# Kernel tuning notes

Measured on AMD Instinct MI355X. Metric: run time of the kernel, lower is better.

Reference implementation:

```python
import jax, jax.numpy as jnp
import numpy as np

CH = (64, 128, 256, 512)
KV = sum(CH)          # 960, kv_size = sum(channel_num)
EPS = 1e-5            # InstanceNorm2d default eps
SCALE = 1.0 / float(np.sqrt(KV))


def setup_inputs() -> dict:
    key = jax.random.key(0)
    ks = jax.random.split(key, 16)
    B, N = 16, 1024
    d = {}
    for i, c in enumerate(CH):
        d[f"emb{i+1}"] = jax.random.normal(ks[i], (B, N, c), jnp.float32)
    d["emb_all"] = jax.random.normal(ks[4], (B, N, KV), jnp.float32)
    for i, c in enumerate(CH):
        # two stacked query heads per branch, Linear weights [out,in]
        d[f"Wq{i+1}"] = jax.random.normal(ks[5 + i], (2, c, c), jnp.float32) * 0.05
        d[f"Wo{i+1}"] = jax.random.normal(ks[9 + i], (c, c), jnp.float32) * 0.05
    d["Wk"] = jax.random.normal(ks[13], (2, KV, KV), jnp.float32) * 0.02
    d["Wv"] = jax.random.normal(ks[14], (2, KV, KV), jnp.float32) * 0.02
    return d


def _attend(emb, Wq, Wo, k, v):
    # emb: [B,N,C]; Wq: [H=2,C,C]; k,v: [B,H,N,KV]
    # torch: stack([Linear(emb) for 2 heads], dim=1).transpose(-1,-2) -> [B,H,C,N]
    q = jnp.einsum('bnc,hdc->bhdn', emb, Wq)
    scores = jnp.einsum('bhdn,bhnk->bhdk', q, k) * SCALE          # [B,H,C,KV]
    # InstanceNorm2d over spatial dims (C,KV) per (batch, head); biased var, no affine
    mu = scores.mean(axis=(2, 3), keepdims=True)
    var = scores.var(axis=(2, 3), keepdims=True)
    probs = jax.nn.softmax((scores - mu) * jax.lax.rsqrt(var + EPS), axis=3)
    # context = probs @ v^T -> [B,H,C,N]; permute(0,3,2,1).mean(3) == mean over heads -> [B,N,C]
    ctx = jnp.einsum('bhdk,bhnk->bnd', probs, v) / probs.shape[1]
    return jnp.einsum('bnd,ed->bne', ctx, Wo)                     # out Linear, no bias


def reference(emb1, emb2, emb3, emb4, emb_all,
              Wq1, Wq2, Wq3, Wq4, Wk, Wv, Wo1, Wo2, Wo3, Wo4):
    # shared multi-head key/value from concatenated embedding: [B,H,N,KV]
    k = jnp.einsum('bnk,hmk->bhnm', emb_all, Wk)
    v = jnp.einsum('bnk,hmk->bhnm', emb_all, Wv)
    outs = [_attend(e, Wq, Wo, k, v) for e, Wq, Wo in (
        (emb1, Wq1, Wo1), (emb2, Wq2, Wo2), (emb3, Wq3, Wo3), (emb4, Wq4, Wo4))]
    # outputs (out1..out4) concatenated along channel for a single array result
    return jnp.concatenate(outs, axis=-1)
```

## Files before the change

kernel.cpp:

```cpp
#include <hip/hip_runtime.h>
#include <cmath>

#define B_   16
#define N_   1024
#define KV_  960
#define H_   2
#define LDP  1024
#define PGE  ((size_t)1024 * 1024)

typedef __attribute__((ext_vector_type(8))) short     short8;
typedef __attribute__((ext_vector_type(8))) unsigned short ushort8;
typedef __attribute__((ext_vector_type(4))) unsigned short ushort4v;
typedef __attribute__((ext_vector_type(4))) float     f32x4;
typedef __attribute__((ext_vector_type(4))) float     float4v;
typedef __attribute__((ext_vector_type(2))) float     float2v;

__device__ inline ushort f2b(float f) {
    union { float f; unsigned u; } x; x.f = f;
    unsigned r = x.u + 0x7FFFu + ((x.u >> 16) & 1u);
    return (ushort)(r >> 16);
}
__device__ inline float b2f(ushort u) {
    union { unsigned u; float f; } x; x.u = (unsigned)u << 16; return x.f;
}

__device__ inline int xcd_swz(int orig, int nwg) {
    int q = nwg >> 3, r = nwg & 7;
    int xcd = orig & 7, idx = orig >> 3;
    return (xcd < r ? xcd * (q + 1) : r * (q + 1) + (xcd - r) * q) + idx;
}

__device__ inline void gload16(const ushort* g, ushort* l) {
    __builtin_amdgcn_global_load_lds(
        (const __attribute__((address_space(1))) void*)g,
        (__attribute__((address_space(3))) void*)l, 16, 0, 0);
}

template<int HSUM, bool OUTF32, bool STATS>
__global__ __launch_bounds__(256)
void gemm128(int gx, int gy, int K, float alpha,
             const ushort* __restrict__ A, size_t sAb, size_t sAh,
             const ushort* __restrict__ Bm, size_t sBb, size_t sBh,
             void* __restrict__ C, int ldc, size_t sCb, size_t sCh, int hsel,
             float2v* __restrict__ parts)
{
    __shared__ ushort As[2][128 * 32];
    __shared__ ushort Bs[2][128 * 32];
    const int wgid = xcd_swz(blockIdx.x, gridDim.x);
    const int xg = wgid % gx, rem = wgid / gx;
    const int yg = rem % gy, z = rem / gy;
    int b, h;
    if (hsel >= 0) { b = z; h = hsel; } else { b = z >> 1; h = z & 1; }
    const int m0 = yg * 128, n0 = xg * 128;
    const int t = threadIdx.x, lane = t & 63, wave = t >> 6;
    const int wr = wave >> 1, wc = wave & 1;

    f32x4 acc[4][4];
#pragma unroll
    for (int i = 0; i < 4; ++i)
#pragma unroll
        for (int j = 0; j < 4; ++j) acc[i][j] = f32x4{0.f, 0.f, 0.f, 0.f};

    int srow[2], skof[2];
#pragma unroll
    for (int j = 0; j < 2; ++j) {
        int s = wave * 64 + j * 256 + lane;
        srow[j] = s >> 2;
        skof[j] = ((s & 3) ^ ((srow[j] >> 1) & 3)) * 8;
    }
    int aoff[4], boff[4];
#pragma unroll
    for (int i = 0; i < 4; ++i) {
        int ra = wr * 64 + i * 16 + (lane & 15);
        aoff[i] = ra * 32 + (((lane >> 4) ^ ((ra >> 1) & 3)) * 8);
        int rb = wc * 64 + i * 16 + (lane & 15);
        boff[i] = rb * 32 + (((lane >> 4) ^ ((rb >> 1) & 3)) * 8);
    }

    const int ksteps = K >> 5;
    const int total  = HSUM * ksteps;

    auto stage = [&](int s, int buf) {
        const int hh = (HSUM == 2) ? (s >= ksteps ? 1 : 0) : h;
        const int k0 = ((HSUM == 2 && s >= ksteps) ? (s - ksteps) : s) << 5;
        const ushort* Ab = A + (size_t)b * sAb + (size_t)hh * sAh;
        const ushort* Bb = Bm + (size_t)b * sBb + (size_t)hh * sBh;
#pragma unroll
        for (int j = 0; j < 2; ++j) {
            int sbase = wave * 64 + j * 256;
            gload16(Ab + (size_t)(m0 + srow[j]) * LDP + k0 + skof[j], &As[buf][sbase * 8]);
            gload16(Bb + (size_t)(n0 + srow[j]) * LDP + k0 + skof[j], &Bs[buf][sbase * 8]);
        }
    };

    stage(0, 0);
    __syncthreads();
    int cur = 0;
    for (int s = 0; s < total; ++s) {
        if (s + 1 < total) stage(s + 1, cur ^ 1);
        short8 a[4], bv[4];
#pragma unroll
        for (int i = 0; i < 4; ++i) {
            a[i]  = *(const short8*)&As[cur][aoff[i]];
            bv[i] = *(const short8*)&Bs[cur][boff[i]];
        }
#pragma unroll
        for (int i = 0; i < 4; ++i)
#pragma unroll
            for (int j = 0; j < 4; ++j)
                acc[i][j] = __builtin_amdgcn_mfma_f32_16x16x32_bf16(a[i], bv[j], acc[i][j], 0, 0, 0);
        __syncthreads();
        cur ^= 1;
    }

    char* Cb = (char*)C + ((size_t)b * sCb + (size_t)h * sCh) * (OUTF32 ? 4 : 2);
#pragma unroll
    for (int i = 0; i < 4; ++i) {
        int row = m0 + wr * 64 + i * 16 + (lane >> 4) * 4;
#pragma unroll
        for (int q = 0; q < 4; ++q)
#pragma unroll
            for (int j = 0; j < 4; ++j) {
                int col = n0 + wc * 64 + j * 16 + (lane & 15);
                float v = alpha * acc[i][j][q];
                if (OUTF32) ((float*)Cb)[(size_t)(row + q) * ldc + col] = v;
                else        ((ushort*)Cb)[(size_t)(row + q) * ldc + col] = f2b(v);
            }
    }

    if constexpr (STATS) {
        float s1[4] = {0.f, 0.f, 0.f, 0.f}, s2[4] = {0.f, 0.f, 0.f, 0.f};
#pragma unroll
        for (int i = 0; i < 4; ++i) {
            int row = m0 + wr * 64 + i * 16 + (lane >> 4) * 4;
#pragma unroll
            for (int q = 0; q < 4; ++q) {
                int rr = row + q;
                if (rr >= KV_) continue;
                int br = rr < 64 ? 0 : rr < 192 ? 1 : rr < 448 ? 2 : 3;
#pragma unroll
                for (int j = 0; j < 4; ++j) {
                    int col = n0 + wc * 64 + j * 16 + (lane & 15);
                    if (col >= KV_) continue;
                    float v = alpha * acc[i][j][q];
                    s1[br] += v; s2[br] += v * v;
                }
            }
        }
#pragma unroll
        for (int br = 0; br < 4; ++br)
#pragma unroll
            for (int o = 32; o; o >>= 1) {
                s1[br] += __shfl_down(s1[br], o);
                s2[br] += __shfl_down(s2[br], o);
            }
        __shared__ float red[4][8];
        if (lane == 0) {
#pragma unroll
            for (int br = 0; br < 4; ++br) { red[wave][br] = s1[br]; red[wave][4 + br] = s2[br]; }
        }
        __syncthreads();
        if (t < 4) {
            float S1 = red[0][t] + red[1][t] + red[2][t] + red[3][t];
            float S2 = red[0][4 + t] + red[1][4 + t] + red[2][4 + t] + red[3][4 + t];
            float2v r; r[0] = S1; r[1] = S2;
            parts[((size_t)z * 64 + yg * 8 + xg) * 4 + t] = r;
        }
    }
}

__device__ inline void stage64b(const ushort* __restrict__ src, int ld, int r0, int k0,
                                ushort* __restrict__ lds, int t)
{
#pragma unroll
    for (int rep = 0; rep < 2; ++rep) {
        int idx = t + rep * 256;
        int rr = idx >> 3, kc = (idx & 7) << 3;
        *(ushort8*)&lds[rr * 72 + kc] =
            *(const ushort8*)(src + (size_t)(r0 + rr) * ld + (k0 + kc));
    }
}

__global__ __launch_bounds__(256)
void ygemm(const ushort* __restrict__ W0, const ushort* __restrict__ W1,
           const ushort* __restrict__ W2, const ushort* __restrict__ W3,
           const ushort* __restrict__ G2, ushort* __restrict__ Y)
{
    __shared__ ushort As[64 * 72];
    __shared__ ushort Bs[64 * 72];
    const int wg = xcd_swz(blockIdx.x, gridDim.x);
    const int z = wg / 225, tl = wg % 225;
    const int b = z >> 1, h = z & 1;
    const int br = tl < 15 ? 0 : tl < 45 ? 1 : tl < 105 ? 2 : 3;
    const int st = br == 0 ? 0 : br == 1 ? 15 : br == 2 ? 45 : 105;
    const int loc = tl - st;
    const int xg = loc % 15, yg = loc / 15;
    const int csz[4]  = {64, 128, 256, 512};
    const int coff[4] = {0, 64, 192, 448};
    const ushort* wp[4] = {W0, W1, W2, W3};
    const int c = csz[br];
    const ushort* A = wp[br] + (size_t)h * c * c;
    const ushort* B = G2 + (size_t)b * PGE + coff[br];
    ushort* Cp = Y + (size_t)b * 2 * PGE + (size_t)h * PGE + (size_t)coff[br] * LDP;
    const int m0 = yg * 64, n0 = xg * 64;
    const int t = threadIdx.x, lane = t & 63, wave = t >> 6;
    const int wr = wave >> 1, wc = wave & 1;

    f32x4 z4 = {0.f, 0.f, 0.f, 0.f};
    f32x4 acc[2][2]; acc[0][0] = z4; acc[0][1] = z4; acc[1][0] = z4; acc[1][1] = z4;

    for (int k0 = 0; k0 < c; k0 += 64) {
        stage64b(A, c, m0, k0, As, t);
        stage64b(B, LDP, n0, k0, Bs, t);
        __syncthreads();
        const int ar = wr * 32 + (lane & 15);
        const int brw = wc * 32 + (lane & 15);
        const int kg = (lane >> 4) * 8;
#pragma unroll
        for (int ks = 0; ks < 2; ++ks) {
            short8 a0 = *(const short8*)&As[(ar)      * 72 + ks * 32 + kg];
            short8 a1 = *(const short8*)&As[(ar + 16) * 72 + ks * 32 + kg];
            short8 b0 = *(const short8*)&Bs[(brw)      * 72 + ks * 32 + kg];
            short8 b1 = *(const short8*)&Bs[(brw + 16) * 72 + ks * 32 + kg];
            acc[0][0] = __builtin_amdgcn_mfma_f32_16x16x32_bf16(a0, b0, acc[0][0], 0, 0, 0);
            acc[0][1] = __builtin_amdgcn_mfma_f32_16x16x32_bf16(a0, b1, acc[0][1], 0, 0, 0);
            acc[1][0] = __builtin_amdgcn_mfma_f32_16x16x32_bf16(a1, b0, acc[1][0], 0, 0, 0);
            acc[1][1] = __builtin_amdgcn_mfma_f32_16x16x32_bf16(a1, b1, acc[1][1], 0, 0, 0);
        }
        __syncthreads();
    }
#pragma unroll
    for (int i = 0; i < 2; ++i)
#pragma unroll
        for (int q = 0; q < 4; ++q) {
            int row = m0 + wr * 32 + i * 16 + (lane >> 4) * 4 + q;
#pragma unroll
            for (int j = 0; j < 2; ++j) {
                int col = n0 + wc * 32 + j * 16 + (lane & 15);
                Cp[(size_t)row * LDP + col] = f2b(acc[i][j][q]);
            }
        }
}

__global__ __launch_bounds__(256)
void ogemm(const ushort* __restrict__ ctx,
           const ushort* __restrict__ O0, const ushort* __restrict__ O1,
           const ushort* __restrict__ O2, const ushort* __restrict__ O3,
           float* __restrict__ out)
{
    __shared__ ushort As[64 * 72];
    __shared__ ushort Bs[64 * 72];
    const int wg = xcd_swz(blockIdx.x, gridDim.x);
    const int b = wg / 240, tl = wg % 240;
    const int br = tl < 16 ? 0 : tl < 48 ? 1 : tl < 112 ? 2 : 3;
    const int st = br == 0 ? 0 : br == 1 ? 16 : br == 2 ? 48 : 112;
    const int loc = tl - st;
    const int csz[4]  = {64, 128, 256, 512};
    const int coff[4] = {0, 64, 192, 448};
    const ushort* op[4] = {O0, O1, O2, O3};
    const int c = csz[br];
    const int gxi = c / 64;
    const int xg = loc % gxi, yg = loc / gxi;
    const ushort* A = ctx + (size_t)b * PGE + coff[br];
    const ushort* B = op[br];
    float* Cf = out + (size_t)b * ((size_t)N_ * KV_) + coff[br];
    const int m0 = yg * 64, n0 = xg * 64;
    const int t = threadIdx.x, lane = t & 63, wave = t >> 6;
    const int wr = wave >> 1, wc = wave & 1;

    f32x4 z4 = {0.f, 0.f, 0.f, 0.f};
    f32x4 acc[2][2]; acc[0][0] = z4; acc[0][1] = z4; acc[1][0] = z4; acc[1][1] = z4;

    for (int k0 = 0; k0 < c; k0 += 64) {
        stage64b(A, LDP, m0, k0, As, t);
        stage64b(B, c, n0, k0, Bs, t);
        __syncthreads();
        const int ar = wr * 32 + (lane & 15);
        const int brw = wc * 32 + (lane & 15);
        const int kg = (lane >> 4) * 8;
#pragma unroll
        for (int ks = 0; ks < 2; ++ks) {
            short8 a0 = *(const short8*)&As[(ar)      * 72 + ks * 32 + kg];
            short8 a1 = *(const short8*)&As[(ar + 16) * 72 + ks * 32 + kg];
            short8 b0 = *(const short8*)&Bs[(brw)      * 72 + ks * 32 + kg];
            short8 b1 = *(const short8*)&Bs[(brw + 16) * 72 + ks * 32 + kg];
            acc[0][0] = __builtin_amdgcn_mfma_f32_16x16x32_bf16(a0, b0, acc[0][0], 0, 0, 0);
            acc[0][1] = __builtin_amdgcn_mfma_f32_16x16x32_bf16(a0, b1, acc[0][1], 0, 0, 0);
            acc[1][0] = __builtin_amdgcn_mfma_f32_16x16x32_bf16(a1, b0, acc[1][0], 0, 0, 0);
            acc[1][1] = __builtin_amdgcn_mfma_f32_16x16x32_bf16(a1, b1, acc[1][1], 0, 0, 0);
        }
        __syncthreads();
    }
#pragma unroll
    for (int i = 0; i < 2; ++i)
#pragma unroll
        for (int q = 0; q < 4; ++q) {
            int row = m0 + wr * 32 + i * 16 + (lane >> 4) * 4 + q;
#pragma unroll
            for (int j = 0; j < 2; ++j) {
                int col = n0 + wc * 32 + j * 16 + (lane & 15);
                Cf[(size_t)row * KV_ + col] = acc[i][j][q];
            }
        }
}

struct WSeg { const float* s; ushort* d; unsigned n; };
struct WcvtA { WSeg seg[8]; };
__global__ __launch_bounds__(256)
void wcvt(WcvtA a)
{
    WSeg sg = a.seg[blockIdx.y];
    for (size_t i = ((size_t)blockIdx.x * 256 + threadIdx.x) * 4; i < sg.n;
         i += (size_t)gridDim.x * 1024) {
        float4v f = *(const float4v*)(sg.s + i);
        ushort4v v;
        v[0] = f2b(f[0]); v[1] = f2b(f[1]); v[2] = f2b(f[2]); v[3] = f2b(f[3]);
        *(ushort4v*)(sg.d + i) = v;
    }
}

__global__ __launch_bounds__(256)
void cvt_ld(const float* __restrict__ src, int sld, ushort* __restrict__ dst,
            int dld, int total_chunks)
{
    for (int ch = blockIdx.x * 256 + threadIdx.x; ch < total_chunks;
         ch += gridDim.x * 256) {
        int row = ch / 120, c = (ch % 120) * 8;
        const float* s = src + (size_t)row * sld + c;
        float4v f0 = *(const float4v*)s;
        float4v f1 = *(const float4v*)(s + 4);
        ushort8 v;
        v[0] = f2b(f0[0]); v[1] = f2b(f0[1]); v[2] = f2b(f0[2]); v[3] = f2b(f0[3]);
        v[4] = f2b(f1[0]); v[5] = f2b(f1[1]); v[6] = f2b(f1[2]); v[7] = f2b(f1[3]);
        *(ushort8*)(dst + (size_t)row * dld + c) = v;
    }
}

__global__ __launch_bounds__(256)
void tposecvt(const float* __restrict__ src, size_t sSrc, int sld,
              ushort* __restrict__ dst, size_t sDst, int dld)
{
    __shared__ ushort tile[32][33];
    const float* s = src + (size_t)blockIdx.z * sSrc;
    ushort* d = dst + (size_t)blockIdx.z * sDst;
    int c0 = blockIdx.x * 32, r0 = blockIdx.y * 32;
    for (int i = threadIdx.y; i < 32; i += 8)
        tile[i][threadIdx.x] = f2b(s[(size_t)(r0 + i) * sld + c0 + threadIdx.x]);
    __syncthreads();
    for (int i = threadIdx.y; i < 32; i += 8)
        d[(size_t)(c0 + i) * dld + r0 + threadIdx.x] = tile[threadIdx.x][i];
}

__global__ __launch_bounds__(256)
void embtall(const float* __restrict__ e0, const float* __restrict__ e1,
             const float* __restrict__ e2, const float* __restrict__ e3,
             ushort* __restrict__ embT)
{
    __shared__ ushort tile[32][33];
    const int xt = blockIdx.x;
    const int br = xt < 2 ? 0 : xt < 6 ? 1 : xt < 14 ? 2 : 3;
    const int st = br == 0 ? 0 : br == 1 ? 2 : br == 2 ? 6 : 14;
    const int loc = xt - st;
    const int csz[4]  = {64, 128, 256, 512};
    const int coff[4] = {0, 64, 192, 448};
    const float* ep[4] = {e0, e1, e2, e3};
    const int c = csz[br];
    const float* s = ep[br] + (size_t)blockIdx.z * ((size_t)N_ * c);
    ushort* d = embT + (size_t)blockIdx.z * (2 * PGE) + (size_t)coff[br] * LDP;
    int c0 = loc * 32, r0 = blockIdx.y * 32;
    for (int i = threadIdx.y; i < 32; i += 8)
        tile[i][threadIdx.x] = f2b(s[(size_t)(r0 + i) * c + c0 + threadIdx.x]);
    __syncthreads();
    for (int i = threadIdx.y; i < 32; i += 8)
        d[(size_t)(c0 + i) * LDP + r0 + threadIdx.x] = tile[threadIdx.x][i];
}

__global__ __launch_bounds__(256)
void dualcvt(const float* __restrict__ src, ushort* __restrict__ ea, size_t sEA,
             ushort* __restrict__ eat, size_t sEAT)
{
    __shared__ ushort tile[32][33];
    const float* s = src + (size_t)blockIdx.z * ((size_t)N_ * KV_);
    ushort* pea  = ea  + (size_t)blockIdx.z * sEA;
    ushort* peat = eat + (size_t)blockIdx.z * sEAT;
    int m0 = blockIdx.x * 32, n0 = blockIdx.y * 32;
    for (int i = threadIdx.y; i < 32; i += 8) {
        ushort bv = f2b(s[(size_t)(n0 + i) * KV_ + m0 + threadIdx.x]);
        tile[i][threadIdx.x] = bv;
        pea[(size_t)(n0 + i) * LDP + m0 + threadIdx.x] = bv;
    }
    __syncthreads();
    for (int i = threadIdx.y; i < 32; i += 8)
        peat[(size_t)(m0 + i) * LDP + n0 + threadIdx.x] = tile[threadIdx.x][i];
}

__global__ __launch_bounds__(64)
void normstats2b(const float2v* __restrict__ parts, float* __restrict__ stats)
{
    const int z = blockIdx.x;
    const int bh = z >> 2, br = z & 3;
    const int csz[4] = {64, 128, 256, 512};
    if (threadIdx.x == 0) {
        float s = 0.f, s2 = 0.f;
        const float2v* p = parts + (size_t)bh * 256 + br;
        for (int t = 0; t < 64; ++t) {
            float2v r = p[t * 4];
            s += r[0]; s2 += r[1];
        }
        const float inv_cnt = 1.0f / (float)(csz[br] * KV_);
        float mu  = s * inv_cnt;
        float var = s2 * inv_cnt - mu * mu;
        stats[2 * z]     = mu;
        stats[2 * z + 1] = rsqrtf(var + 1e-5f);
    }
}

__global__ __launch_bounds__(256)
void psoftmax(ushort* __restrict__ S, const float* __restrict__ stats)
{
    const int r  = blockIdx.x;
    const int bh  = r / KV_;
    const int row = r % KV_;
    const int br  = (row < 64) ? 0 : (row < 192) ? 1 : (row < 448) ? 2 : 3;
    const float mu = stats[2 * (bh * 4 + br)];
    const float rs = stats[2 * (bh * 4 + br) + 1];
    ushort* p = S + (size_t)bh * PGE + (size_t)row * LDP;

    const int t = threadIdx.x;
    float x[4];
    float mx = -1e30f;
#pragma unroll
    for (int i = 0; i < 4; ++i) {
        int idx = t + i * 256;
        x[i] = (idx < KV_) ? (b2f(p[idx]) - mu) * rs : -1e30f;
        mx = fmaxf(mx, x[i]);
    }
#pragma unroll
    for (int o = 1; o < 64; o <<= 1) mx = fmaxf(mx, __shfl_xor(mx, o));
    __shared__ float wmax[4], wsum[4];
    int w = t >> 6, l = t & 63;
    if (l == 0) wmax[w] = mx;
    __syncthreads();
    mx = fmaxf(fmaxf(wmax[0], wmax[1]), fmaxf(wmax[2], wmax[3]));

    float s = 0.f;
#pragma unroll
    for (int i = 0; i < 4; ++i) {
        x[i] = expf(x[i] - mx);
        s += x[i];
    }
#pragma unroll
    for (int o = 1; o < 64; o <<= 1) s += __shfl_xor(s, o);
    if (l == 0) wsum[w] = s;
    __syncthreads();
    s = wsum[0] + wsum[1] + wsum[2] + wsum[3];
    float inv = 1.0f / s;
#pragma unroll
    for (int i = 0; i < 4; ++i) {
        int idx = t + i * 256;
        if (idx < KV_) p[idx] = f2b(x[i] * inv);
    }
}

extern "C" void kernel_launch(void* const* d_in, const int* in_sizes, int n_in,
                              void* d_out, int out_size, void* d_ws, size_t ws_size,
                              hipStream_t stream)
{
    const float* emb[4] = {(const float*)d_in[0], (const float*)d_in[1],
                           (const float*)d_in[2], (const float*)d_in[3]};
    const float* emb_all = (const float*)d_in[4];
    const float* Wq[4] = {(const float*)d_in[5], (const float*)d_in[7],
                          (const float*)d_in[9], (const float*)d_in[11]};
    const float* Wo[4] = {(const float*)d_in[6], (const float*)d_in[8],
                          (const float*)d_in[10], (const float*)d_in[12]};
    const float* Wk = (const float*)d_in[13];
    const float* Wv = (const float*)d_in[14];
    float* out = (float*)d_out;

    const int c_sz[4]  = {64, 128, 256, 512};
    const int c_off[4] = {0, 64, 192, 448};

    const size_t BN  = (size_t)N_ * KV_;
    const size_t GE9 = (size_t)KV_ * KV_;
    const float SCALE = 0.03227486121839514f;

    char* wsp = (char*)d_ws;
    size_t off = 0;
    auto alloc = [&](size_t bytes) -> char* {
        off = (off + 255) & ~(size_t)255;
        char* p = wsp + off;
        off += bytes;
        return p;
    };

    ushort* WqB[4]; ushort* WoB[4];
    for (int i = 0; i < 4; ++i) WqB[i] = (ushort*)alloc((size_t)2 * c_sz[i] * c_sz[i] * 2);
    for (int i = 0; i < 4; ++i) WoB[i] = (ushort*)alloc((size_t)c_sz[i] * c_sz[i] * 2);
    ushort* WkB = (ushort*)alloc(2 * PGE * 2);
    ushort* WvT = (ushort*)alloc(2 * PGE * 2);

    {
        WcvtA a;
        for (int i = 0; i < 4; ++i) {
            a.seg[i]     = { Wq[i], WqB[i], (unsigned)(2 * c_sz[i] * c_sz[i]) };
            a.seg[4 + i] = { Wo[i], WoB[i], (unsigned)(c_sz[i] * c_sz[i]) };
        }
        wcvt<<<dim3(64, 8), 256, 0, stream>>>(a);
    }
    for (int hh = 0; hh < 2; ++hh)
        cvt_ld<<<dim3(450), 256, 0, stream>>>(Wk + hh * GE9, KV_, WkB + hh * PGE, LDP, 960 * 120);
    tposecvt<<<dim3(30, 30, 2), dim3(32, 8), 0, stream>>>(Wv, GE9, KV_, WvT, PGE, LDP);

    const size_t perB = 6 * PGE * 2;
    size_t statik = (off + 255) & ~(size_t)255;
    int NB = 16;
    while (NB > 1 && statik + (size_t)NB * perB + 262144 > ws_size) NB >>= 1;

    ushort* slotA = (ushort*)alloc((size_t)NB * PGE * 2);
    ushort* Y     = (ushort*)alloc((size_t)NB * 2 * PGE * 2);
    ushort* Sc    = (ushort*)alloc((size_t)NB * 2 * PGE * 2);
    ushort* EA    = (ushort*)alloc((size_t)NB * PGE * 2);
    float*  stats = (float*) alloc((size_t)NB * 2 * 4 * 2 * 4);
    float2v* parts = (float2v*)alloc((size_t)NB * 2 * 64 * 4 * 8);
    ushort* EAT  = Sc;
    ushort* embT = Y;
    ushort* R    = Y;

    for (int b0 = 0; b0 < B_; b0 += NB) {
        dualcvt<<<dim3(30, 32, NB), dim3(32, 8), 0, stream>>>(
            emb_all + (size_t)b0 * BN, EA, PGE, EAT, 2 * PGE);
        embtall<<<dim3(30, 32, NB), dim3(32, 8), 0, stream>>>(
            emb[0] + (size_t)b0 * N_ * 64,  emb[1] + (size_t)b0 * N_ * 128,
            emb[2] + (size_t)b0 * N_ * 256, emb[3] + (size_t)b0 * N_ * 512,
            embT);

        gemm128<1, false, false><<<dim3(8 * 8 * NB), 256, 0, stream>>>(
            8, 8, N_, 1.0f,
            EAT, 2 * PGE, 0,
            embT, 2 * PGE, 0,
            slotA, LDP, PGE, 0, 0, nullptr);

        ygemm<<<dim3(NB * 2 * 225), 256, 0, stream>>>(
            WqB[0], WqB[1], WqB[2], WqB[3], slotA, Y);

        gemm128<1, false, true><<<dim3(8 * 8 * NB * H_), 256, 0, stream>>>(
            8, 8, KV_, SCALE,
            Y, 2 * PGE, PGE,
            WkB, 0, PGE,
            Sc, LDP, 2 * PGE, PGE, -1, parts);

        normstats2b<<<NB * H_ * 4, 64, 0, stream>>>(parts, stats);
        psoftmax<<<NB * H_ * KV_, 256, 0, stream>>>(Sc, stats);

        gemm128<2, false, false><<<dim3(8 * 8 * NB), 256, 0, stream>>>(
            8, 8, KV_, 1.0f,
            Sc, 2 * PGE, PGE,
            WvT, 0, PGE,
            R, LDP, 2 * PGE, 0, 0, nullptr);

        gemm128<1, false, false><<<dim3(8 * 8 * NB), 256, 0, stream>>>(
            8, 8, KV_, 0.5f,
            EA, PGE, 0,
            R, 2 * PGE, 0,
            slotA, LDP, PGE, 0, 0, nullptr);

        ogemm<<<dim3(NB * 240), 256, 0, stream>>>(
            slotA, WoB[0], WoB[1], WoB[2], WoB[3],
            out + (size_t)b0 * BN);
    }
}
```

Before: 523.8 us.

## Unroll GEMM pipeline by two, widen transpose tiles, merge Wk conversion launches

The GEMM main loop is unrolled by two with fixed buffer indices, and the per-head base pointers are hoisted out of the staging lambda to cut address arithmetic. The transpose/convert kernels for emb_all and the branch embeddings now use 64x64 float tiles with 64-wide thread rows, aiming for wider coalesced accesses and fewer blocks. The two Wk conversion launches are merged into one 2D grid. The float LDS tiles raise shared-memory use per block, and the 64-wide ushort stores are still narrow.

New measurement: 533.8 us. Within noise of the previous version (+1.9%).

```diff
diff --git a/kernel.cpp b/kernel.cpp
--- a/kernel.cpp
+++ b/kernel.cpp
@@ -80,11 +80,17 @@
     const int ksteps = K >> 5;
     const int total  = HSUM * ksteps;
 
+    const ushort* AbH0 = A  + (size_t)b * sAb + (size_t)((HSUM == 2) ? 0 : h) * sAh;
+    const ushort* BbH0 = Bm + (size_t)b * sBb + (size_t)((HSUM == 2) ? 0 : h) * sBh;
+    const ushort* AbH1 = A  + (size_t)b * sAb + sAh;
+    const ushort* BbH1 = Bm + (size_t)b * sBb + sBh;
+
     auto stage = [&](int s, int buf) {
-        const int hh = (HSUM == 2) ? (s >= ksteps ? 1 : 0) : h;
-        const int k0 = ((HSUM == 2 && s >= ksteps) ? (s - ksteps) : s) << 5;
-        const ushort* Ab = A + (size_t)b * sAb + (size_t)hh * sAh;
-        const ushort* Bb = Bm + (size_t)b * sBb + (size_t)hh * sBh;
+        const ushort* Ab; const ushort* Bb; int k0;
+        if constexpr (HSUM == 2) {
+            if (s >= ksteps) { Ab = AbH1; Bb = BbH1; k0 = (s - ksteps) << 5; }
+            else             { Ab = AbH0; Bb = BbH0; k0 = s << 5; }
+        } else { Ab = AbH0; Bb = BbH0; k0 = s << 5; }
 #pragma unroll
         for (int j = 0; j < 2; ++j) {
             int sbase = wave * 64 + j * 256;
@@ -93,24 +99,38 @@
         }
     };
 
+    auto compute = [&](int buf) {
+        short8 a[4], bv[4];
+#pragma unroll
+        for (int i = 0; i < 4; ++i) {
+            a[i]  = *(const short8*)&As[buf][aoff[i]];
+            bv[i] = *(const short8*)&Bs[buf][boff[i]];
+        }
+#pragma unroll
+        for (int i = 0; i < 4; ++i)
+#pragma unroll
+            for (int j = 0; j < 4; ++j)
+                acc[i][j] = __builtin_amdgcn_mfma_f32_16x16x32_bf16(a[i], bv[j], acc[i][j], 0, 0, 0);
+    };
+
     stage(0, 0);
     __syncthreads();
-    int cur = 0;
-    for (int s = 0; s < total; ++s) {
-        if (s + 1 < total) stage(s + 1, cur ^ 1);
-        short8 a[4], bv[4];
-#pragma unroll
-        for (int i = 0; i < 4; ++i) {
-            a[i]  = *(const short8*)&As[cur][aoff[i]];
-            bv[i] = *(const short8*)&Bs[cur][boff[i]];
-        }
-#pragma unroll
-        for (int i = 0; i < 4; ++i)
-#pragma unroll
-            for (int j = 0; j < 4; ++j)
-                acc[i][j] = __builtin_amdgcn_mfma_f32_16x16x32_bf16(a[i], bv[j], acc[i][j], 0, 0, 0);
-        __syncthreads();
-        cur ^= 1;
+    int s = 0;
+    for (; s + 2 < total; s += 2) {
+        stage(s + 1, 1);
+        compute(0);
+        __syncthreads();
+        stage(s + 2, 0);
+        compute(1);
+        __syncthreads();
+    }
+    if (total - s == 2) {
+        stage(s + 1, 1);
+        compute(0);
+        __syncthreads();
+        compute(1);
+    } else {
+        compute(0);
     }
 
     char* Cb = (char*)C + ((size_t)b * sCb + (size_t)h * sCh) * (OUTF32 ? 4 : 2);
@@ -320,19 +340,21 @@
 }
 
 __global__ __launch_bounds__(256)
-void cvt_ld(const float* __restrict__ src, int sld, ushort* __restrict__ dst,
-            int dld, int total_chunks)
-{
+void cvt_ld(const float* __restrict__ src, int sld, size_t sYsrc,
+            ushort* __restrict__ dst, int dld, size_t sYdst, int total_chunks)
+{
+    const float* s0 = src + (size_t)blockIdx.y * sYsrc;
+    ushort* d0 = dst + (size_t)blockIdx.y * sYdst;
     for (int ch = blockIdx.x * 256 + threadIdx.x; ch < total_chunks;
          ch += gridDim.x * 256) {
         int row = ch / 120, c = (ch % 120) * 8;
-        const float* s = src + (size_t)row * sld + c;
+        const float* s = s0 + (size_t)row * sld + c;
         float4v f0 = *(const float4v*)s;
         float4v f1 = *(const float4v*)(s + 4);
         ushort8 v;
         v[0] = f2b(f0[0]); v[1] = f2b(f0[1]); v[2] = f2b(f0[2]); v[3] = f2b(f0[3]);
         v[4] = f2b(f1[0]); v[5] = f2b(f1[1]); v[6] = f2b(f1[2]); v[7] = f2b(f1[3]);
-        *(ushort8*)(dst + (size_t)row * dld + c) = v;
+        *(ushort8*)(d0 + (size_t)row * dld + c) = v;
     }
 }
 
@@ -352,14 +374,34 @@
 }
 
 __global__ __launch_bounds__(256)
+void dualcvt(const float* __restrict__ src, ushort* __restrict__ ea, size_t sEA,
+             ushort* __restrict__ eat, size_t sEAT)
+{
+    __shared__ float tile[64][65];
+    const float* s = src + (size_t)blockIdx.z * ((size_t)N_ * KV_);
+    ushort* pea  = ea  + (size_t)blockIdx.z * sEA;
+    ushort* peat = eat + (size_t)blockIdx.z * sEAT;
+    int m0 = blockIdx.x * 64, n0 = blockIdx.y * 64;
+    int tx = threadIdx.x, ty = threadIdx.y;
+    for (int i = ty; i < 64; i += 4) {
+        float v = s[(size_t)(n0 + i) * KV_ + m0 + tx];
+        tile[i][tx] = v;
+        pea[(size_t)(n0 + i) * LDP + m0 + tx] = f2b(v);
+    }
+    __syncthreads();
+    for (int i = ty; i < 64; i += 4)
+        peat[(size_t)(m0 + i) * LDP + n0 + tx] = f2b(tile[tx][i]);
+}
+
+__global__ __launch_bounds__(256)
 void embtall(const float* __restrict__ e0, const float* __restrict__ e1,
              const float* __restrict__ e2, const float* __restrict__ e3,
              ushort* __restrict__ embT)
 {
-    __shared__ ushort tile[32][33];
+    __shared__ float tile[64][65];
     const int xt = blockIdx.x;
-    const int br = xt < 2 ? 0 : xt < 6 ? 1 : xt < 14 ? 2 : 3;
-    const int st = br == 0 ? 0 : br == 1 ? 2 : br == 2 ? 6 : 14;
+    const int br = xt < 1 ? 0 : xt < 3 ? 1 : xt < 7 ? 2 : 3;
+    const int st = br == 0 ? 0 : br == 1 ? 1 : br == 2 ? 3 : 7;
     const int loc = xt - st;
     const int csz[4]  = {64, 128, 256, 512};
     const int coff[4] = {0, 64, 192, 448};
@@ -367,31 +409,13 @@
     const int c = csz[br];
     const float* s = ep[br] + (size_t)blockIdx.z * ((size_t)N_ * c);
     ushort* d = embT + (size_t)blockIdx.z * (2 * PGE) + (size_t)coff[br] * LDP;
-    int c0 = loc * 32, r0 = blockIdx.y * 32;
-    for (int i = threadIdx.y; i < 32; i += 8)
-        tile[i][threadIdx.x] = f2b(s[(size_t)(r0 + i) * c + c0 + threadIdx.x]);
+    int c0 = loc * 64, r0 = blockIdx.y * 64;
+    int tx = threadIdx.x, ty = threadIdx.y;
+    for (int i = ty; i < 64; i += 4)
+        tile[i][tx] = s[(size_t)(r0 + i) * c + c0 + tx];
     __syncthreads();
-    for (int i = threadIdx.y; i < 32; i += 8)
-        d[(size_t)(c0 + i) * LDP + r0 + threadIdx.x] = tile[threadIdx.x][i];
-}
-
-__global__ __launch_bounds__(256)
-void dualcvt(const float* __restrict__ src, ushort* __restrict__ ea, size_t sEA,
-             ushort* __restrict__ eat, size_t sEAT)
-{
-    __shared__ ushort tile[32][33];
-    const float* s = src + (size_t)blockIdx.z * ((size_t)N_ * KV_);
-    ushort* pea  = ea  + (size_t)blockIdx.z * sEA;
-    ushort* peat = eat + (size_t)blockIdx.z * sEAT;
-    int m0 = blockIdx.x * 32, n0 = blockIdx.y * 32;
-    for (int i = threadIdx.y; i < 32; i += 8) {
-        ushort bv = f2b(s[(size_t)(n0 + i) * KV_ + m0 + threadIdx.x]);
-        tile[i][threadIdx.x] = bv;
-        pea[(size_t)(n0 + i) * LDP + m0 + threadIdx.x] = bv;
-    }
-    __syncthreads();
-    for (int i = threadIdx.y; i < 32; i += 8)
-        peat[(size_t)(m0 + i) * LDP + n0 + threadIdx.x] = tile[threadIdx.x][i];
+    for (int i = ty; i < 64; i += 4)
+        d[(size_t)(c0 + i) * LDP + r0 + tx] = f2b(tile[tx][i]);
 }
 
 __global__ __launch_bounds__(64)
@@ -478,7 +502,6 @@
     float* out = (float*)d_out;
 
     const int c_sz[4]  = {64, 128, 256, 512};
-    const int c_off[4] = {0, 64, 192, 448};
 
     const size_t BN  = (size_t)N_ * KV_;
     const size_t GE9 = (size_t)KV_ * KV_;
@@ -507,8 +530,7 @@
         }
         wcvt<<<dim3(64, 8), 256, 0, stream>>>(a);
     }
-    for (int hh = 0; hh < 2; ++hh)
-        cvt_ld<<<dim3(450), 256, 0, stream>>>(Wk + hh * GE9, KV_, WkB + hh * PGE, LDP, 960 * 120);
+    cvt_ld<<<dim3(450, 2), 256, 0, stream>>>(Wk, KV_, GE9, WkB, LDP, PGE, 960 * 120);
     tposecvt<<<dim3(30, 30, 2), dim3(32, 8), 0, stream>>>(Wv, GE9, KV_, WvT, PGE, LDP);
 
     const size_t perB = 6 * PGE * 2;
@@ -527,9 +549,9 @@
     ushort* R    = Y;
 
     for (int b0 = 0; b0 < B_; b0 += NB) {
-        dualcvt<<<dim3(30, 32, NB), dim3(32, 8), 0, stream>>>(
+        dualcvt<<<dim3(15, 16, NB), dim3(64, 4), 0, stream>>>(
             emb_all + (size_t)b0 * BN, EA, PGE, EAT, 2 * PGE);
-        embtall<<<dim3(30, 32, NB), dim3(32, 8), 0, stream>>>(
+        embtall<<<dim3(15, 16, NB), dim3(64, 4), 0, stream>>>(
             emb[0] + (size_t)b0 * N_ * 64,  emb[1] + (size_t)b0 * N_ * 128,
             emb[2] + (size_t)b0 * N_ * 256, emb[3] + (size_t)b0 * N_ * 512,
             embT);
```
